# Kernel tuning notes

Hardware: AMD Instinct MI355X
Metric: run time of the kernel (lower is better)

## Reference

```python
import jax, jax.numpy as jnp
import numpy as np

EMBED = 1024
HEADS = 16
HEAD_DIM = EMBED // HEADS


def setup_inputs() -> dict:
    key = jax.random.key(0)
    k1, k2, k3 = jax.random.split(key, 3)
    hidden_states = jax.random.normal(k1, (2, 2048, EMBED), dtype=jnp.float32)
    # Conv1D weights are stored (nx, nf): y = x @ W + b
    c_attn_w = jax.random.normal(k2, (EMBED, 3 * EMBED), dtype=jnp.float32) * 0.02
    c_attn_b = jnp.zeros((3 * EMBED,), dtype=jnp.float32)
    c_proj_w = jax.random.normal(k3, (EMBED, EMBED), dtype=jnp.float32) * 0.02
    c_proj_b = jnp.zeros((EMBED,), dtype=jnp.float32)
    return {
        "hidden_states": hidden_states,
        "c_attn_w": c_attn_w,
        "c_attn_b": c_attn_b,
        "c_proj_w": c_proj_w,
        "c_proj_b": c_proj_b,
    }


def reference(hidden_states, c_attn_w, c_attn_b, c_proj_w, c_proj_b):
    B, S, E = hidden_states.shape
    H, D = HEADS, HEAD_DIM
    fused = hidden_states @ c_attn_w + c_attn_b  # [B,S,3E]
    q, k, v = jnp.split(fused, 3, axis=-1)
    # split heads -> [B,H,S,D]
    q = q.reshape(B, S, H, D).transpose(0, 2, 1, 3)
    k = k.reshape(B, S, H, D).transpose(0, 2, 1, 3)
    v = v.reshape(B, S, H, D).transpose(0, 2, 1, 3)
    scores = jnp.einsum("bhqd,bhkd->bhqk", q, k) / jnp.sqrt(jnp.float32(D))
    probs = jax.nn.softmax(scores, axis=-1)  # NOTE: no causal mask in source
    attn = jnp.einsum("bhqk,bhkd->bhqd", probs, v)
    out = attn.transpose(0, 2, 1, 3).reshape(B, S, E)
    return out @ c_proj_w + c_proj_b
```

## Files before the change

### kernel.cpp

```cpp
#include <hip/hip_runtime.h>
#include <hip/hip_bf16.h>
#include <cstdint>
#include <cstddef>

#define E_ 1024
#define H_ 16
#define D_ 64
#define B_ 2
#define S_ 2048
#define T_ 4096
#define NQ_ 3072

typedef __bf16 bf16_t;
typedef bf16_t bf16x8 __attribute__((ext_vector_type(8)));
typedef float f32x4 __attribute__((ext_vector_type(4)));

static __device__ __forceinline__ unsigned short f2bf(float f) {
    __hip_bfloat16 h = __float2bfloat16(f);
    return __builtin_bit_cast(unsigned short, h);
}
static __device__ __forceinline__ unsigned cvt_pk(float a, float b) {
    unsigned r;
    asm("v_cvt_pk_bf16_f32 %0, %1, %2" : "=v"(r) : "v"(a), "v"(b));
    return r;
}
static __device__ __forceinline__ bf16x8 ld_frag(const unsigned short* p) {
    uint4 u = *reinterpret_cast<const uint4*>(p);
    return __builtin_bit_cast(bf16x8, u);
}
static __device__ __forceinline__ void cp16(unsigned short* lds, const unsigned short* g) {
    __builtin_amdgcn_global_load_lds(
        (const __attribute__((address_space(1))) unsigned int*)g,
        (__attribute__((address_space(3))) unsigned int*)lds, 16, 0, 0);
}
static __device__ __forceinline__ f32x4 mfma16(bf16x8 a, bf16x8 b, f32x4 c) {
    return __builtin_amdgcn_mfma_f32_16x16x32_bf16(a, b, c, 0, 0, 0);
}

__global__ __launch_bounds__(256) void k_wt2(
    const float* __restrict__ w1, unsigned short* __restrict__ w1t,
    const float* __restrict__ w2, unsigned short* __restrict__ w2t)
{
    __shared__ float tbuf[32][33];
    const float* in;
    unsigned short* out;
    int N, bx;
    if (blockIdx.x < 96) { in = w1; out = w1t; N = NQ_; bx = blockIdx.x; }
    else                 { in = w2; out = w2t; N = E_;  bx = blockIdx.x - 96; }
    int n0 = bx * 32, k0 = blockIdx.y * 32;
    int tx = threadIdx.x, ty = threadIdx.y;
    for (int j = 0; j < 4; j++) {
        int r = ty + j * 8;
        tbuf[r][tx] = in[(size_t)(k0 + r) * N + n0 + tx];
    }
    __syncthreads();
    for (int j = 0; j < 4; j++) {
        int r = ty + j * 8;
        out[(size_t)(n0 + r) * E_ + k0 + tx] = f2bf(tbuf[tx][r]);
    }
}

__global__ __launch_bounds__(256) void k_qkv(
    const float* __restrict__ Hs, const unsigned short* __restrict__ Wt,
    const float* __restrict__ bias,
    unsigned short* __restrict__ Qb, unsigned short* __restrict__ Kb,
    unsigned short* __restrict__ Vb)
{
    __shared__ __attribute__((aligned(16))) unsigned short As[128 * 32];
    __shared__ __attribute__((aligned(16))) unsigned short Bs[128 * 32];

    const int t = threadIdx.x;
    const int w = t >> 6, lane = t & 63, lr = lane & 15, lq = lane >> 4;
    const int wm = (w >> 1) * 64, wn = (w & 1) * 64;
    const int m0 = blockIdx.x * 128, n0 = blockIdx.y * 128;

    f32x4 acc[4][4];
    for (int mt = 0; mt < 4; mt++)
        for (int nt = 0; nt < 4; nt++)
            acc[mt][nt] = (f32x4){0.f, 0.f, 0.f, 0.f};

    for (int kt = 0; kt < E_; kt += 32) {
        __syncthreads();
        for (int i = 0; i < 2; i++) {
            int c = t + i * 256;
            int row = c >> 2, kp = (c & 3) * 8;
            cp16(&Bs[c * 8], &Wt[(size_t)(n0 + row) * E_ + kt + kp]);
        }
        for (int i = 0; i < 4; i++) {
            int c = t + i * 256;
            int row = c >> 3, k4 = (c & 7) * 4;
            float4 v = *reinterpret_cast<const float4*>(&Hs[(size_t)(m0 + row) * E_ + kt + k4]);
            uint2 o;
            o.x = cvt_pk(v.x, v.y);
            o.y = cvt_pk(v.z, v.w);
            *reinterpret_cast<uint2*>(&As[row * 32 + k4]) = o;
        }
        __syncthreads();
        bf16x8 af[4], bfr[4];
        for (int mt = 0; mt < 4; mt++) af[mt]  = ld_frag(&As[(wm + mt * 16 + lr) * 32 + lq * 8]);
        for (int nt = 0; nt < 4; nt++) bfr[nt] = ld_frag(&Bs[(wn + nt * 16 + lr) * 32 + lq * 8]);
        for (int mt = 0; mt < 4; mt++)
            for (int nt = 0; nt < 4; nt++)
                acc[mt][nt] = mfma16(af[mt], bfr[nt], acc[mt][nt]);
    }

    const int sector = (n0 >> 10);
    for (int nt = 0; nt < 4; nt++) {
        int n = n0 + wn + nt * 16 + lr;
        float bv = bias[n];
        int nn = n & 1023, h = nn >> 6, d = nn & 63;
        for (int mt = 0; mt < 4; mt++) {
            for (int i = 0; i < 4; i++) {
                int tok = m0 + wm + mt * 16 + lq * 4 + i;
                int b = tok >> 11, s = tok & 2047;
                float v = acc[mt][nt][i] + bv;
                if (sector == 0) {
                    Qb[(((size_t)(b * H_ + h) * S_ + s) << 6) + d] = f2bf(v * 0.18033688f);
                } else if (sector == 1) {
                    Kb[(((size_t)(b * H_ + h) * S_ + s) << 6) + d] = f2bf(v);
                } else {
                    Vb[(((size_t)(b * H_ + h) * D_ + d) << 11) + s] = f2bf(v);
                }
            }
        }
    }
}

__global__ __launch_bounds__(256) void k_attn(
    const unsigned short* __restrict__ Qb, const unsigned short* __restrict__ Kb,
    const unsigned short* __restrict__ Vb, unsigned short* __restrict__ Ob)
{
    __shared__ __attribute__((aligned(16))) unsigned short Ks[2][128 * 64];
    __shared__ __attribute__((aligned(16))) unsigned short Vt[2][64 * 128];
    __shared__ __attribute__((aligned(16))) unsigned short Ps[4][32 * 64];

    const int t = threadIdx.x, w = t >> 6, lane = t & 63, lr = lane & 15, lq = lane >> 4;
    const int h = blockIdx.y, b = blockIdx.z;
    const size_t head = ((size_t)(b * H_ + h)) * (S_ * D_);
    const unsigned short* Qh = Qb + head;
    const unsigned short* Kh = Kb + head;
    const unsigned short* Vh = Vb + head;
    const int q0 = blockIdx.x * 128 + w * 16;
    const int swz = lr & 7;

    bf16x8 qa[2][2];
    for (int qh = 0; qh < 2; qh++)
        for (int kk = 0; kk < 2; kk++)
            qa[qh][kk] = ld_frag(&Qh[(size_t)(q0 + qh * 64 + lr) * 64 + kk * 32 + lq * 8]);

    f32x4 o[2][4];
    for (int qh = 0; qh < 2; qh++)
        for (int i = 0; i < 4; i++) o[qh][i] = (f32x4){0.f, 0.f, 0.f, 0.f};
    float lsum[2] = {0.f, 0.f};
    unsigned short* Pw = Ps[w];

    auto stage = [&](int bb, int kt) {
        for (int i = 0; i < 4; i++) {
            int c = t + i * 256;
            int row = c >> 3, sp = c & 7;
            cp16(&Ks[bb][c * 8], &Kh[(size_t)(kt + row) * 64 + (sp ^ (row & 7)) * 8]);
        }
        for (int i = 0; i < 4; i++) {
            int c = t + i * 256;
            int d = c >> 4, sp = c & 15, seg = (sp & 8) | ((sp & 7) ^ (d & 7));
            cp16(&Vt[bb][c * 8], &Vh[(size_t)d * S_ + kt + seg * 8]);
        }
    };

    stage(0, 0);
    asm volatile("s_waitcnt vmcnt(0)" ::: "memory");
    __syncthreads();

    int cur = 0;
#pragma unroll 2
    for (int kt = 0; kt < S_; kt += 128) {
        if (kt + 128 < S_) stage(cur ^ 1, kt + 128);

        const unsigned short* Kc = Ks[cur];
        const unsigned short* Vc = Vt[cur];

#pragma unroll
        for (int ss = 0; ss < 2; ss++) {
            for (int tau = 0; tau < 4; tau++) {
                int krow = ss * 64 + tau * 16 + lr;
                bf16x8 kf0 = ld_frag(&Kc[krow * 64 + ((0 + lq) ^ swz) * 8]);
                bf16x8 kf1 = ld_frag(&Kc[krow * 64 + ((4 + lq) ^ swz) * 8]);
                for (int qh = 0; qh < 2; qh++) {
                    f32x4 z = (f32x4){0.f, 0.f, 0.f, 0.f};
                    __builtin_amdgcn_s_setprio(1);
                    z = mfma16(kf0, qa[qh][0], z);
                    z = mfma16(kf1, qa[qh][1], z);
                    __builtin_amdgcn_s_setprio(0);
                    float e0 = __builtin_amdgcn_exp2f(z[0]);
                    float e1 = __builtin_amdgcn_exp2f(z[1]);
                    float e2 = __builtin_amdgcn_exp2f(z[2]);
                    float e3 = __builtin_amdgcn_exp2f(z[3]);
                    lsum[qh] += (e0 + e1) + (e2 + e3);
                    uint2 pk;
                    pk.x = cvt_pk(e0, e1);
                    pk.y = cvt_pk(e2, e3);
                    int seg = (tau * 2 + (lq >> 1)) ^ swz;
                    *reinterpret_cast<uint2*>(&Pw[(qh * 16 + lr) * 64 + seg * 8 + (lq & 1) * 4]) = pk;
                }
            }
            for (int kk = 0; kk < 2; kk++) {
                bf16x8 pf0 = ld_frag(&Pw[(lr) * 64 + ((kk * 4 + lq) ^ swz) * 8]);
                bf16x8 pf1 = ld_frag(&Pw[(16 + lr) * 64 + ((kk * 4 + lq) ^ swz) * 8]);
                __builtin_amdgcn_s_setprio(1);
                for (int t2 = 0; t2 < 4; t2++) {
                    int vrow = t2 * 16 + lr;
                    bf16x8 vf = ld_frag(&Vc[vrow * 128 + ((ss * 8) | ((kk * 4 + lq) ^ swz)) * 8]);
                    o[0][t2] = mfma16(vf, pf0, o[0][t2]);
                    o[1][t2] = mfma16(vf, pf1, o[1][t2]);
                }
                __builtin_amdgcn_s_setprio(0);
            }
        }

        asm volatile("s_waitcnt vmcnt(0)" ::: "memory");
        __syncthreads();
        cur ^= 1;
    }

    for (int qh = 0; qh < 2; qh++) {
        float ls = lsum[qh];
        ls += __shfl_xor(ls, 16, 64);
        ls += __shfl_xor(ls, 32, 64);
        float inv = 1.0f / ls;

        int s = q0 + qh * 64 + lr;
        size_t rowoff = ((size_t)(b * S_ + s)) * E_ + h * 64;
        for (int t2 = 0; t2 < 4; t2++) {
            uint2 pk;
            pk.x = cvt_pk(o[qh][t2][0] * inv, o[qh][t2][1] * inv);
            pk.y = cvt_pk(o[qh][t2][2] * inv, o[qh][t2][3] * inv);
            *reinterpret_cast<uint2*>(&Ob[rowoff + t2 * 16 + lq * 4]) = pk;
        }
    }
}

__global__ __launch_bounds__(256) void k_proj(
    const unsigned short* __restrict__ Ab, const unsigned short* __restrict__ Wt,
    const float* __restrict__ bias, float* __restrict__ out)
{
    __shared__ __attribute__((aligned(16))) unsigned short As[128 * 32];
    __shared__ __attribute__((aligned(16))) unsigned short Bs[64 * 32];
    const int t = threadIdx.x;
    const int w = t >> 6, lane = t & 63, lr = lane & 15, lq = lane >> 4;
    const int wm = (w >> 1) * 64, wn = (w & 1) * 32;
    const int m0 = blockIdx.x * 128, n0 = blockIdx.y * 64;

    f32x4 acc[4][2];
    for (int mt = 0; mt < 4; mt++)
        for (int nt = 0; nt < 2; nt++)
            acc[mt][nt] = (f32x4){0.f, 0.f, 0.f, 0.f};

    for (int kt = 0; kt < E_; kt += 32) {
        __syncthreads();
        for (int i = 0; i < 2; i++) {
            int c = t + i * 256;
            int row = c >> 2, kp = (c & 3) * 8;
            cp16(&As[c * 8], &Ab[(size_t)(m0 + row) * E_ + kt + kp]);
        }
        {
            int c = t;
            int row = c >> 2, kp = (c & 3) * 8;
            cp16(&Bs[c * 8], &Wt[(size_t)(n0 + row) * E_ + kt + kp]);
        }
        __syncthreads();
        bf16x8 af[4], bfr[2];
        for (int mt = 0; mt < 4; mt++) af[mt]  = ld_frag(&As[(wm + mt * 16 + lr) * 32 + lq * 8]);
        for (int nt = 0; nt < 2; nt++) bfr[nt] = ld_frag(&Bs[(wn + nt * 16 + lr) * 32 + lq * 8]);
        for (int mt = 0; mt < 4; mt++)
            for (int nt = 0; nt < 2; nt++)
                acc[mt][nt] = mfma16(af[mt], bfr[nt], acc[mt][nt]);
    }

    for (int nt = 0; nt < 2; nt++) {
        int n = n0 + wn + nt * 16 + lr;
        float bv = bias[n];
        for (int mt = 0; mt < 4; mt++)
            for (int i = 0; i < 4; i++) {
                int tok = m0 + wm + mt * 16 + lq * 4 + i;
                out[(size_t)tok * E_ + n] = acc[mt][nt][i] + bv;
            }
    }
}

extern "C" void kernel_launch(void* const* d_in, const int* in_sizes, int n_in,
                              void* d_out, int out_size, void* d_ws, size_t ws_size,
                              hipStream_t stream) {
    const float* hs = (const float*)d_in[0];
    const float* w1 = (const float*)d_in[1];
    const float* b1 = (const float*)d_in[2];
    const float* w2 = (const float*)d_in[3];
    const float* b2 = (const float*)d_in[4];
    float* out = (float*)d_out;

    char* ws = (char*)d_ws;
    unsigned short* w1t = (unsigned short*)(ws + (size_t)( 8 << 20));
    unsigned short* w2t = (unsigned short*)(ws + (size_t)(14 << 20));
    unsigned short* Qb  = (unsigned short*)(ws + (size_t)(16 << 20));
    unsigned short* Kb  = (unsigned short*)(ws + (size_t)(24 << 20));
    unsigned short* Vb  = (unsigned short*)(ws + (size_t)(32 << 20));
    unsigned short* Ao  = (unsigned short*)(ws + (size_t)(40 << 20));

    k_wt2<<<dim3(128, 32), dim3(32, 8), 0, stream>>>(w1, w1t, w2, w2t);
    k_qkv<<<dim3(T_ / 128, NQ_ / 128), dim3(256), 0, stream>>>(hs, w1t, b1, Qb, Kb, Vb);
    k_attn<<<dim3(S_ / 128, H_, B_), dim3(256), 0, stream>>>(Qb, Kb, Vb, Ao);
    k_proj<<<dim3(T_ / 128, E_ / 64), dim3(256), 0, stream>>>(Ao, w2t, b2, out);
}
```

Baseline: 190.3 us.

## Pre-convert activations to bf16 and stage V transpose through LDS

The hidden-state fp32→bf16 conversion moves out of the QKV GEMM into the prep kernel, which also transposes the weights. The GEMM can then load A tiles with direct global-to-LDS copies instead of per-iteration float4 loads and conversions. The V-sector epilogue now transposes through shared memory so V is written as contiguous 16-byte rows instead of scattered 2-byte stores. The cost is an extra 16 MB bf16 activation round trip through memory and a larger shared-memory footprint in the GEMM.

After: 196.5 us. +3.3%, slower.

```diff
diff --git a/kernel.cpp b/kernel.cpp
--- a/kernel.cpp
+++ b/kernel.cpp
@@ -37,18 +37,30 @@
     return __builtin_amdgcn_mfma_f32_16x16x32_bf16(a, b, c, 0, 0, 0);
 }
 
-__global__ __launch_bounds__(256) void k_wt2(
+__global__ __launch_bounds__(256) void k_prep(
+    const float* __restrict__ hs, unsigned short* __restrict__ hb,
     const float* __restrict__ w1, unsigned short* __restrict__ w1t,
     const float* __restrict__ w2, unsigned short* __restrict__ w2t)
 {
+    if (blockIdx.x < 4096) {
+        int i = (blockIdx.x * 256 + threadIdx.x) * 4;
+        float4 v = *reinterpret_cast<const float4*>(hs + i);
+        uint2 o;
+        o.x = cvt_pk(v.x, v.y);
+        o.y = cvt_pk(v.z, v.w);
+        *reinterpret_cast<uint2*>(hb + i) = o;
+        return;
+    }
     __shared__ float tbuf[32][33];
+    int wid = blockIdx.x - 4096;
+    int bx = wid & 127, by = wid >> 7;
     const float* in;
     unsigned short* out;
-    int N, bx;
-    if (blockIdx.x < 96) { in = w1; out = w1t; N = NQ_; bx = blockIdx.x; }
-    else                 { in = w2; out = w2t; N = E_;  bx = blockIdx.x - 96; }
-    int n0 = bx * 32, k0 = blockIdx.y * 32;
-    int tx = threadIdx.x, ty = threadIdx.y;
+    int N;
+    if (bx < 96) { in = w1; out = w1t; N = NQ_; }
+    else         { in = w2; out = w2t; N = E_; bx -= 96; }
+    int n0 = bx * 32, k0 = by * 32;
+    int tx = threadIdx.x & 31, ty = threadIdx.x >> 5;
     for (int j = 0; j < 4; j++) {
         int r = ty + j * 8;
         tbuf[r][tx] = in[(size_t)(k0 + r) * N + n0 + tx];
@@ -61,13 +73,14 @@
 }
 
 __global__ __launch_bounds__(256) void k_qkv(
-    const float* __restrict__ Hs, const unsigned short* __restrict__ Wt,
+    const unsigned short* __restrict__ Ab, const unsigned short* __restrict__ Wt,
     const float* __restrict__ bias,
     unsigned short* __restrict__ Qb, unsigned short* __restrict__ Kb,
     unsigned short* __restrict__ Vb)
 {
-    __shared__ __attribute__((aligned(16))) unsigned short As[128 * 32];
-    __shared__ __attribute__((aligned(16))) unsigned short Bs[128 * 32];
+    __shared__ __attribute__((aligned(16))) unsigned short smem[16896];
+    unsigned short* As = smem;
+    unsigned short* Bs = smem + 4096;
 
     const int t = threadIdx.x;
     const int w = t >> 6, lane = t & 63, lr = lane & 15, lq = lane >> 4;
@@ -84,16 +97,12 @@
         for (int i = 0; i < 2; i++) {
             int c = t + i * 256;
             int row = c >> 2, kp = (c & 3) * 8;
+            cp16(&As[c * 8], &Ab[(size_t)(m0 + row) * E_ + kt + kp]);
+        }
+        for (int i = 0; i < 2; i++) {
+            int c = t + i * 256;
+            int row = c >> 2, kp = (c & 3) * 8;
             cp16(&Bs[c * 8], &Wt[(size_t)(n0 + row) * E_ + kt + kp]);
-        }
-        for (int i = 0; i < 4; i++) {
-            int c = t + i * 256;
-            int row = c >> 3, k4 = (c & 7) * 4;
-            float4 v = *reinterpret_cast<const float4*>(&Hs[(size_t)(m0 + row) * E_ + kt + k4]);
-            uint2 o;
-            o.x = cvt_pk(v.x, v.y);
-            o.y = cvt_pk(v.z, v.w);
-            *reinterpret_cast<uint2*>(&As[row * 32 + k4]) = o;
         }
         __syncthreads();
         bf16x8 af[4], bfr[4];
@@ -105,23 +114,49 @@
     }
 
     const int sector = (n0 >> 10);
-    for (int nt = 0; nt < 4; nt++) {
-        int n = n0 + wn + nt * 16 + lr;
-        float bv = bias[n];
-        int nn = n & 1023, h = nn >> 6, d = nn & 63;
-        for (int mt = 0; mt < 4; mt++) {
-            for (int i = 0; i < 4; i++) {
-                int tok = m0 + wm + mt * 16 + lq * 4 + i;
-                int b = tok >> 11, s = tok & 2047;
-                float v = acc[mt][nt][i] + bv;
-                if (sector == 0) {
-                    Qb[(((size_t)(b * H_ + h) * S_ + s) << 6) + d] = f2bf(v * 0.18033688f);
-                } else if (sector == 1) {
-                    Kb[(((size_t)(b * H_ + h) * S_ + s) << 6) + d] = f2bf(v);
-                } else {
-                    Vb[(((size_t)(b * H_ + h) * D_ + d) << 11) + s] = f2bf(v);
+    if (sector != 2) {
+        for (int nt = 0; nt < 4; nt++) {
+            int n = n0 + wn + nt * 16 + lr;
+            float bv = bias[n];
+            int nn = n & 1023, h = nn >> 6, d = nn & 63;
+            for (int mt = 0; mt < 4; mt++) {
+                for (int i = 0; i < 4; i++) {
+                    int tok = m0 + wm + mt * 16 + lq * 4 + i;
+                    int b = tok >> 11, s = tok & 2047;
+                    float v = acc[mt][nt][i] + bv;
+                    if (sector == 0) {
+                        Qb[(((size_t)(b * H_ + h) * S_ + s) << 6) + d] = f2bf(v * 0.18033688f);
+                    } else {
+                        Kb[(((size_t)(b * H_ + h) * S_ + s) << 6) + d] = f2bf(v);
+                    }
                 }
             }
+        }
+    } else {
+        __syncthreads();
+        for (int nt = 0; nt < 4; nt++) {
+            int nl = wn + nt * 16 + lr;
+            float bv = bias[n0 + nl];
+            unsigned short* vr = &smem[nl * 132];
+            for (int mt = 0; mt < 4; mt++) {
+                int tokb = wm + mt * 16 + lq * 4;
+                uint2 pk;
+                pk.x = cvt_pk(acc[mt][nt][0] + bv, acc[mt][nt][1] + bv);
+                pk.y = cvt_pk(acc[mt][nt][2] + bv, acc[mt][nt][3] + bv);
+                *reinterpret_cast<uint2*>(&vr[tokb]) = pk;
+            }
+        }
+        __syncthreads();
+        int row = t >> 1, half = t & 1;
+        int hglob = ((n0 & 1023) >> 6) + (row >> 6), d = row & 63;
+        int b = m0 >> 11, sbase = (m0 & 2047) + half * 64;
+        size_t gb = (((size_t)(b * H_ + hglob) * D_ + d) << 11) + sbase;
+        const unsigned short* src = &smem[row * 132 + half * 64];
+        for (int jj = 0; jj < 8; jj++) {
+            uint2 a = *reinterpret_cast<const uint2*>(&src[jj * 8]);
+            uint2 bq = *reinterpret_cast<const uint2*>(&src[jj * 8 + 4]);
+            uint4 o4; o4.x = a.x; o4.y = a.y; o4.z = bq.x; o4.w = bq.y;
+            *reinterpret_cast<uint4*>(&Vb[gb + jj * 8]) = o4;
         }
     }
 }
@@ -298,6 +333,7 @@
     float* out = (float*)d_out;
 
     char* ws = (char*)d_ws;
+    unsigned short* hb  = (unsigned short*)(ws);
     unsigned short* w1t = (unsigned short*)(ws + (size_t)( 8 << 20));
     unsigned short* w2t = (unsigned short*)(ws + (size_t)(14 << 20));
     unsigned short* Qb  = (unsigned short*)(ws + (size_t)(16 << 20));
@@ -305,8 +341,8 @@
     unsigned short* Vb  = (unsigned short*)(ws + (size_t)(32 << 20));
     unsigned short* Ao  = (unsigned short*)(ws + (size_t)(40 << 20));
 
-    k_wt2<<<dim3(128, 32), dim3(32, 8), 0, stream>>>(w1, w1t, w2, w2t);
-    k_qkv<<<dim3(T_ / 128, NQ_ / 128), dim3(256), 0, stream>>>(hs, w1t, b1, Qb, Kb, Vb);
+    k_prep<<<dim3(4096 + 4096), dim3(256), 0, stream>>>(hs, hb, w1, w1t, w2, w2t);
+    k_qkv<<<dim3(T_ / 128, NQ_ / 128), dim3(256), 0, stream>>>(hb, w1t, b1, Qb, Kb, Vb);
     k_attn<<<dim3(S_ / 128, H_, B_), dim3(256), 0, stream>>>(Qb, Kb, Vb, Ao);
     k_proj<<<dim3(T_ / 128, E_ / 64), dim3(256), 0, stream>>>(Ao, w2t, b2, out);
 }
```
